# Performance work log

Measured on AMD Instinct MI355X. Metric: run time of the kernel, lower is better.

## Reference

```python
import jax, jax.numpy as jnp
import numpy as np

NIBBLES_PER_I32 = 8


def unpack_int4(q):
    """Unpack int32 [..., n] -> uint4 values in int32 [..., n*8], LSB-first."""
    shifts = (jnp.arange(NIBBLES_PER_I32, dtype=jnp.int32) * 4)
    nib = (q[..., None] >> shifts) & 0xF  # [..., n, 8]
    return nib.reshape(q.shape[:-1] + (q.shape[-1] * NIBBLES_PER_I32,))


def setup_inputs() -> dict:
    key = jax.random.key(0)
    k_x, k_w, k_z, k_s, k_b = jax.random.split(key, 5)
    B, S, IN, OUT, G = 2, 4096, 4096, 4096, 32
    x = jax.random.normal(k_x, (B, S, IN), dtype=jnp.float16)
    qweight = jax.random.randint(k_w, (OUT, IN // 8), 0, 2147483647, dtype=jnp.int32)
    qzeros = jax.random.randint(k_z, (G, OUT // 8), 0, 2147483647, dtype=jnp.int32)
    scales = (jax.random.uniform(k_s, (G, OUT), dtype=jnp.float32) * 0.01 + 0.001).astype(jnp.float16)
    bias = (jax.random.normal(k_b, (OUT,), dtype=jnp.float32) * 0.01).astype(jnp.float16)
    return {"x": x, "qweight": qweight, "qzeros": qzeros, "scales": scales, "bias": bias}


def reference(x, qweight, qzeros, scales, bias):
    # GPTQ W4A16: dequantize int4 weight with per-group scales/zero-points, then GEMM + bias.
    x = x.astype(jnp.float16)
    wq = unpack_int4(qweight)            # [out, in] int4 values
    zq = unpack_int4(qzeros)             # [groups, out]
    out_f, in_f = wq.shape
    G = scales.shape[0]
    gsize = in_f // G
    wq_g = wq.reshape(out_f, G, gsize)                       # [out, G, gsize]
    zero = zq.T.astype(jnp.float16)[:, :, None]              # [out, G, 1]
    scale = scales.T.astype(jnp.float16)[:, :, None]         # [out, G, 1]
    w = ((wq_g.astype(jnp.float16) - zero) * scale).reshape(out_f, in_f)  # [out, in] fp16
    y = jnp.einsum("bsi,oi->bso", x, w)                     # [B, S, out]
    return y + bias
```

## Files before the change

### kernel.cpp

```cpp
#include <hip/hip_runtime.h>
#include <cstdint>

typedef unsigned short u16;
typedef unsigned int   u32;
typedef unsigned long long u64;

typedef _Float16 f16x2 __attribute__((ext_vector_type(2)));
typedef _Float16 f16x8 __attribute__((ext_vector_type(8)));
typedef float    f32x4 __attribute__((ext_vector_type(4)));

__device__ __forceinline__ u32 cvt_pk(float a, float b) {
    return __builtin_bit_cast(u32, __builtin_amdgcn_cvt_pkrtz(a, b));
}

__device__ __forceinline__ f16x8 unpack_dq(u32 q, f16x2 cz, f16x2 cs) {
    const u32 b0 = (q & 0x000F000Fu) | 0x64006400u;
    const u32 b1 = ((q >> 4) & 0x000F000Fu) | 0x64006400u;
    const u32 b2 = ((q >> 8) & 0x000F000Fu) | 0x64006400u;
    const u32 b3 = ((q >> 12) & 0x000F000Fu) | 0x64006400u;
    const f16x2 w0 = (__builtin_bit_cast(f16x2, b0) - cz) * cs;
    const f16x2 w1 = (__builtin_bit_cast(f16x2, b1) - cz) * cs;
    const f16x2 w2 = (__builtin_bit_cast(f16x2, b2) - cz) * cs;
    const f16x2 w3 = (__builtin_bit_cast(f16x2, b3) - cz) * cs;
    uint4 w;
    w.x = __builtin_bit_cast(u32, w0);
    w.y = __builtin_bit_cast(u32, w1);
    w.z = __builtin_bit_cast(u32, w2);
    w.w = __builtin_bit_cast(u32, w3);
    return __builtin_bit_cast(f16x8, w);
}

__device__ __forceinline__ void load_lds16(const void* g, void* l) {
    __builtin_amdgcn_global_load_lds(
        (const __attribute__((address_space(1))) void*)g,
        (__attribute__((address_space(3))) void*)l,
        16, 0, 0);
}

__global__ __launch_bounds__(256) void gptq_prepass(
    const float* __restrict__ X, u16* __restrict__ Xh)
{
    const u32 tile = blockIdx.x;
    const u32 mt = tile >> 6, t = tile & 63;
    const float* bsrc = X + ((u64)mt << 19) + t * 64;
    u16* bdst = Xh + ((u64)tile << 13);
#pragma unroll
    for (int pass = 0; pass < 4; ++pass) {
        const u32 idx = pass * 256 + threadIdx.x;
        const u32 r = idx >> 3, sg = idx & 7, g = sg ^ (r & 7);
        const float* s = bsrc + ((u64)r << 12) + g * 8;
        const float4 f0 = *(const float4*)s;
        const float4 f1 = *(const float4*)(s + 4);
        uint4 w;
        w.x = cvt_pk(f0.x, f1.x);
        w.y = cvt_pk(f0.y, f1.y);
        w.z = cvt_pk(f0.z, f1.z);
        w.w = cvt_pk(f0.w, f1.w);
        *(uint4*)(bdst + idx * 8) = w;
    }
}

__global__ __launch_bounds__(256, 2) void gptq_gemm_dma(
    const u16* __restrict__ Xh,
    const int* __restrict__ QW,
    const int* __restrict__ QZ,
    const float* __restrict__ SC,
    const float* __restrict__ BIAS,
    float* __restrict__ Y)
{
    constexpr int N = 4096, KB = 512, NT = 64;

    __shared__ __align__(16) u16 Alds[2][128 * 64];

    const int tid  = threadIdx.x;
    const int lane = tid & 63;
    const int wid  = tid >> 6;

    const int mt = blockIdx.x;
    const int m0 = mt * 128;
    const int n0 = blockIdx.y * 256;

    f32x4 acc[8][4];
#pragma unroll
    for (int i = 0; i < 8; i++)
#pragma unroll
        for (int j = 0; j < 4; j++)
            acc[i][j] = (f32x4){0.f, 0.f, 0.f, 0.f};

    const int fr   = lane & 15;
    const int quad = lane >> 4;
    const int fr7  = fr & 7;

    const char* xsrc = (const char*)Xh + (((u64)mt * NT) << 14)
                     + wid * 4096 + lane * 16;

    const int nbase = n0 + wid * 64 + fr;
    const char* QWb = (const char*)QW;
    u32 qoff[4];
#pragma unroll
    for (int ni = 0; ni < 4; ni++)
        qoff[ni] = (u32)(((nbase + ni * 16) * KB + quad) * 4);
    const int zsh = fr7 * 4;

    int   bq[2][8];
    float sf_st[4];
    int   zw_st[4];
    f16x2 cs[4], cz[4];

    auto STAGE = [&](int buf, int t) {
        const char* s = xsrc + ((u64)t << 14);
        char* d = (char*)&Alds[buf][0] + wid * 4096;
#pragma unroll
        for (int i = 0; i < 4; i++)
            load_lds16(s + i * 1024, d + i * 1024);
    };

    auto FETCH_B = [&](int t, int nb) {
        const u32 tb = (u32)t * 32;
#pragma unroll
        for (int ni = 0; ni < 4; ni++) {
            bq[nb][ni * 2 + 0] = *(const int*)(QWb + qoff[ni] + tb);
            bq[nb][ni * 2 + 1] = *(const int*)(QWb + qoff[ni] + tb + 16);
        }
    };

    auto FETCH_SZ = [&](int g) {
#pragma unroll
        for (int ni = 0; ni < 4; ni++) {
            sf_st[ni] = SC[g * N + nbase + ni * 16];
            zw_st[ni] = QZ[g * (N / 8) + ((nbase + ni * 16) >> 3)];
        }
    };

    auto CONV_SZ = [&]() {
#pragma unroll
        for (int ni = 0; ni < 4; ni++) {
            const int z = (zw_st[ni] >> zsh) & 0xF;
            const _Float16 hs = (_Float16)sf_st[ni];
            const _Float16 hz = (_Float16)(float)(1024 + z);
            cs[ni] = (f16x2){hs, hs};
            cz[ni] = (f16x2){hz, hz};
        }
    };

    auto COMPUTE = [&](int buf, int nb) {
#pragma unroll
        for (int ks = 0; ks < 2; ks++) {
            f16x8 bfr[4];
#pragma unroll
            for (int ni = 0; ni < 4; ni++)
                bfr[ni] = unpack_dq((u32)bq[nb][ni * 2 + ks], cz[ni], cs[ni]);
            const int gsw = ((ks * 4 + quad) ^ fr7) * 8;
            __builtin_amdgcn_s_setprio(1);
#pragma unroll
            for (int mi = 0; mi < 8; mi++) {
                const f16x8 af =
                    *(const f16x8*)(&Alds[buf][(mi * 16 + fr) * 64 + gsw]);
#pragma unroll
                for (int ni = 0; ni < 4; ni++)
                    acc[mi][ni] = __builtin_amdgcn_mfma_f32_16x16x32_f16(
                        af, bfr[ni], acc[mi][ni], 0, 0, 0);
            }
            __builtin_amdgcn_s_setprio(0);
        }
    };

    FETCH_B(0, 0);
    FETCH_SZ(0);
    STAGE(0, 0);
    STAGE(1, 1);
    CONV_SZ();
    asm volatile("s_waitcnt vmcnt(4)\n\ts_barrier" ::: "memory");

    for (int t = 0; t <= 60; t += 2) {
        FETCH_B(t + 1, 1);
        FETCH_SZ((t >> 1) + 1);
        COMPUTE(0, 0);
        asm volatile("s_barrier" ::: "memory");
        STAGE(0, t + 2);
        asm volatile("s_waitcnt vmcnt(20)\n\ts_barrier" ::: "memory");

        FETCH_B(t + 2, 0);
        COMPUTE(1, 1);
        CONV_SZ();
        asm volatile("s_barrier" ::: "memory");
        STAGE(1, t + 3);
        asm volatile("s_waitcnt vmcnt(12)\n\ts_barrier" ::: "memory");
    }

    FETCH_B(63, 1);
    COMPUTE(0, 0);
    asm volatile("s_waitcnt vmcnt(8)\n\ts_barrier" ::: "memory");
    COMPUTE(1, 1);

    const int cn  = lane & 15;
    const int q4r = quad * 4;
#pragma unroll
    for (int ni = 0; ni < 4; ni++) {
        const int col = n0 + wid * 64 + ni * 16 + cn;
        const float bz = BIAS[col];
#pragma unroll
        for (int mi = 0; mi < 8; mi++) {
            const int rbase = m0 + mi * 16 + q4r;
#pragma unroll
            for (int r = 0; r < 4; r++) {
                Y[(u64)(rbase + r) * N + col] = acc[mi][ni][r] + bz;
            }
        }
    }
}

__global__ __launch_bounds__(256, 2) void gptq_gemm_fb(
    const float* __restrict__ X, const int* __restrict__ QW,
    const int* __restrict__ QZ, const float* __restrict__ SC,
    const float* __restrict__ BIAS, float* __restrict__ Y)
{
    constexpr int N = 4096, K = 4096, KB = 512, NT = 64;
    __shared__ __align__(16) u16 Alds[2][128 * 64];
    __shared__ __align__(16) u16 Blds[2][128 * 64];

    const int tid = threadIdx.x, lane = tid & 63, wid = tid >> 6;
    const int m0 = blockIdx.x * 128, n0 = blockIdx.y * 128;

    f32x4 acc[4][4];
#pragma unroll
    for (int i = 0; i < 4; i++)
#pragma unroll
        for (int j = 0; j < 4; j++) acc[i][j] = (f32x4){0.f, 0.f, 0.f, 0.f};

    const int wm = (wid >> 1) * 64, wn = (wid & 1) * 64;
    const int lrowA = tid >> 3;
    const float* gA = X + (u64)(m0 + lrowA) * K + (tid & 7) * 8;
    const int sA = ((tid & 7) ^ (lrowA & 7)) * 8;
    const int nl = tid >> 1, kq0 = (tid & 1) * 4;
    const int nglob = n0 + nl;
    const int* qrow = QW + (u64)nglob * KB;
    const int nl7 = nl & 7, zsh = (nglob & 7) * 4;
    const float* scp = SC + nglob;
    const int* qzp = QZ + (nglob >> 3);
    const int fr = lane & 15, quad = lane >> 4, fr7 = fr & 7;

    float4 af32[8];
    int4 q4;
    float sf;
    int zw;

    auto FETCH = [&](int t) {
        const int kt = t * 64;
#pragma unroll
        for (int i = 0; i < 4; i++) {
            const float* pa = gA + (u64)i * 32 * K + kt;
            af32[2 * i] = *(const float4*)pa;
            af32[2 * i + 1] = *(const float4*)(pa + 4);
        }
        q4 = *(const int4*)(qrow + (kt >> 3) + kq0);
        const int g = t >> 1;
        sf = scp[g * N];
        zw = qzp[g * (N / 8)];
    };
    auto STORE = [&](int buf) {
#pragma unroll
        for (int i = 0; i < 4; i++) {
            const float4 f0 = af32[2 * i], f1 = af32[2 * i + 1];
            uint4 w;
            w.x = cvt_pk(f0.x, f1.x); w.y = cvt_pk(f0.y, f1.y);
            w.z = cvt_pk(f0.z, f1.z); w.w = cvt_pk(f0.w, f1.w);
            *(uint4*)(&Alds[buf][(i * 32 + lrowA) * 64 + sA]) = w;
        }
        const int z = (zw >> zsh) & 0xF;
        const _Float16 hs = (_Float16)sf;
        const _Float16 hz = (_Float16)(float)(1024 + z);
        const f16x2 cs2 = {hs, hs}, cz2 = {hz, hz};
        const int qv[4] = {q4.x, q4.y, q4.z, q4.w};
#pragma unroll
        for (int c = 0; c < 4; c++) {
            const f16x8 wv = unpack_dq((u32)qv[c], cz2, cs2);
            const int gran = ((kq0 + c) ^ nl7) * 8;
            *(f16x8*)(&Blds[buf][nl * 64 + gran]) = wv;
        }
    };
    auto COMPUTE = [&](int buf) {
#pragma unroll
        for (int ks = 0; ks < 2; ks++) {
            const int gsw = ((ks * 4 + quad) ^ fr7) * 8;
            f16x8 af[4], bfr[4];
#pragma unroll
            for (int i = 0; i < 4; i++)
                af[i] = *(const f16x8*)(&Alds[buf][(wm + i * 16 + fr) * 64 + gsw]);
#pragma unroll
            for (int i = 0; i < 4; i++)
                bfr[i] = *(const f16x8*)(&Blds[buf][(wn + i * 16 + fr) * 64 + gsw]);
#pragma unroll
            for (int mi = 0; mi < 4; mi++)
#pragma unroll
                for (int ni = 0; ni < 4; ni++)
                    acc[mi][ni] = __builtin_amdgcn_mfma_f32_16x16x32_f16(
                        af[mi], bfr[ni], acc[mi][ni], 0, 0, 0);
        }
    };

    FETCH(0); STORE(0); __syncthreads();
#pragma unroll 2
    for (int t = 0; t < NT; ++t) {
        const int cur = t & 1;
        if (t + 1 < NT) FETCH(t + 1);
        COMPUTE(cur);
        if (t + 1 < NT) STORE(cur ^ 1);
        __syncthreads();
    }
    const int cn = lane & 15, q4r = quad * 4;
#pragma unroll
    for (int ni = 0; ni < 4; ni++) {
        const int col = n0 + wn + ni * 16 + cn;
        const float bz = BIAS[col];
#pragma unroll
        for (int mi = 0; mi < 4; mi++) {
            const int rbase = m0 + wm + mi * 16 + q4r;
#pragma unroll
            for (int r = 0; r < 4; r++)
                Y[(u64)(rbase + r) * N + col] = acc[mi][ni][r] + bz;
        }
    }
}

extern "C" void kernel_launch(void* const* d_in, const int* in_sizes, int n_in,
                              void* d_out, int out_size, void* d_ws, size_t ws_size,
                              hipStream_t stream) {
    const float* X    = (const float*)d_in[0];
    const int*   QW   = (const int*)d_in[1];
    const int*   QZ   = (const int*)d_in[2];
    const float* SC   = (const float*)d_in[3];
    const float* BIAS = (const float*)d_in[4];
    float* Y = (float*)d_out;

    const size_t need = (size_t)8192 * 4096 * sizeof(u16);
    if (ws_size >= need) {
        u16* Xh = (u16*)d_ws;
        gptq_prepass<<<4096, 256, 0, stream>>>(X, Xh);
        dim3 grid(64, 16, 1);
        gptq_gemm_dma<<<grid, 256, 0, stream>>>(Xh, QW, QZ, SC, BIAS, Y);
    } else {
        dim3 grid(64, 32, 1);
        gptq_gemm_fb<<<grid, 256, 0, stream>>>(X, QW, QZ, SC, BIAS, Y);
    }
}
```

Measured before the change: 581.1 us.

## Transpose packed int4 weights in a prepass for coalesced GEMM weight loads

Adds a kernel that transposes the packed int4 weight matrix into a K-major layout in workspace each call. The GEMM then reads weights so that adjacent lanes touch adjacent columns, giving coalesced 4-byte loads instead of 2KB-strided scattered loads. It costs an extra launch plus an 8MB read and write per call. It also needs more workspace, and if that is not available the code falls back to the slower kernel.

```diff
diff --git a/kernel.cpp b/kernel.cpp
--- a/kernel.cpp
+++ b/kernel.cpp
@@ -60,15 +60,42 @@
     }
 }
 
+__global__ __launch_bounds__(256) void gptq_transpose(
+    const int* __restrict__ QW, int* __restrict__ QWt)
+{
+    __shared__ int tile[64][65];
+    const u32 bkq = blockIdx.x;
+    const u32 bn  = blockIdx.y;
+    const u32 t = threadIdx.x;
+    const u32 r = t >> 4, c4 = (t & 15) * 4;
+#pragma unroll
+    for (int p = 0; p < 4; ++p) {
+        const u32 row = p * 16 + r;
+        const int4 v = *(const int4*)(QW + (u64)(bn * 64 + row) * 512
+                                         + bkq * 64 + c4);
+        tile[row][c4 + 0] = v.x; tile[row][c4 + 1] = v.y;
+        tile[row][c4 + 2] = v.z; tile[row][c4 + 3] = v.w;
+    }
+    __syncthreads();
+#pragma unroll
+    for (int p = 0; p < 4; ++p) {
+        const u32 kql = p * 16 + r;
+        int4 v;
+        v.x = tile[c4 + 0][kql]; v.y = tile[c4 + 1][kql];
+        v.z = tile[c4 + 2][kql]; v.w = tile[c4 + 3][kql];
+        *(int4*)(QWt + (u64)(bkq * 64 + kql) * 4096 + bn * 64 + c4) = v;
+    }
+}
+
 __global__ __launch_bounds__(256, 2) void gptq_gemm_dma(
     const u16* __restrict__ Xh,
-    const int* __restrict__ QW,
+    const int* __restrict__ QWt,
     const int* __restrict__ QZ,
     const float* __restrict__ SC,
     const float* __restrict__ BIAS,
     float* __restrict__ Y)
 {
-    constexpr int N = 4096, KB = 512, NT = 64;
+    constexpr int N = 4096, NT = 64;
 
     __shared__ __align__(16) u16 Alds[2][128 * 64];
 
@@ -95,17 +122,14 @@
                      + wid * 4096 + lane * 16;
 
     const int nbase = n0 + wid * 64 + fr;
-    const char* QWb = (const char*)QW;
-    u32 qoff[4];
-#pragma unroll
-    for (int ni = 0; ni < 4; ni++)
-        qoff[ni] = (u32)(((nbase + ni * 16) * KB + quad) * 4);
-    const int zsh = fr7 * 4;
+    const char* QWtB = (const char*)QWt;
+    const u64 qtbase = (u64)((u32)(quad * 4096 + nbase) * 4u);
 
     int   bq[2][8];
     float sf_st[4];
     int   zw_st[4];
     f16x2 cs[4], cz[4];
+    const int zsh = fr7 * 4;
 
     auto STAGE = [&](int buf, int t) {
         const char* s = xsrc + ((u64)t << 14);
@@ -116,11 +140,11 @@
     };
 
     auto FETCH_B = [&](int t, int nb) {
-        const u32 tb = (u32)t * 32;
+        const char* p = QWtB + ((u64)t << 17) + qtbase;
 #pragma unroll
         for (int ni = 0; ni < 4; ni++) {
-            bq[nb][ni * 2 + 0] = *(const int*)(QWb + qoff[ni] + tb);
-            bq[nb][ni * 2 + 1] = *(const int*)(QWb + qoff[ni] + tb + 16);
+            bq[nb][ni * 2 + 0] = *(const int*)(p + ni * 64);
+            bq[nb][ni * 2 + 1] = *(const int*)(p + 65536 + ni * 64);
         }
     };
 
@@ -333,12 +357,15 @@
     const float* BIAS = (const float*)d_in[4];
     float* Y = (float*)d_out;
 
-    const size_t need = (size_t)8192 * 4096 * sizeof(u16);
-    if (ws_size >= need) {
-        u16* Xh = (u16*)d_ws;
+    const size_t needXh = (size_t)8192 * 4096 * sizeof(u16);
+    const size_t needAll = needXh + (size_t)512 * 4096 * 4;
+    if (ws_size >= needAll) {
+        u16* Xh  = (u16*)d_ws;
+        int* QWt = (int*)((char*)d_ws + needXh);
         gptq_prepass<<<4096, 256, 0, stream>>>(X, Xh);
+        gptq_transpose<<<dim3(8, 64), 256, 0, stream>>>(QW, QWt);
         dim3 grid(64, 16, 1);
-        gptq_gemm_dma<<<grid, 256, 0, stream>>>(Xh, QW, QZ, SC, BIAS, Y);
+        gptq_gemm_dma<<<grid, 256, 0, stream>>>(Xh, QWt, QZ, SC, BIAS, Y);
     } else {
         dim3 grid(64, 32, 1);
         gptq_gemm_fb<<<grid, 256, 0, stream>>>(X, QW, QZ, SC, BIAS, Y);
```

Result: faster. 480.3 us (-17.3%).
